# Kernel tuning notes

Hardware: AMD Instinct MI355X
Metric: run time of the kernel (lower is better)

Reference implementation:

```python
import jax, jax.numpy as jnp
import numpy as np

GROUPS = 8
EPS = 1e-5


def group_norm_dim1(x, gamma, beta):
    # Faithful to torch: GroupNorm treats dim 1 (height) as the channel axis.
    B, H, W, C = x.shape
    xg = x.reshape(B, GROUPS, H // GROUPS, W, C)
    mean = xg.mean(axis=(2, 3, 4), keepdims=True)
    var = xg.var(axis=(2, 3, 4), keepdims=True)
    xn = ((xg - mean) * jax.lax.rsqrt(var + EPS)).reshape(B, H, W, C)
    return xn * gamma[None, :, None, None] + beta[None, :, None, None]


def setup_inputs() -> dict:
    key = jax.random.key(0)
    ks = jax.random.split(key, 8)
    B, H, W, C = 4, 64, 64, 64  # height must equal units for GroupNorm to apply
    s = 1.0 / np.sqrt(C)
    return {
        "x": jax.random.normal(ks[0], (B, H, W, C), dtype=jnp.float32),
        "gamma": jnp.ones((C,), jnp.float32),
        "beta": jnp.zeros((C,), jnp.float32),
        "Wq": jax.random.normal(ks[1], (C, C), jnp.float32) * s,
        "bq": jnp.zeros((C,), jnp.float32),
        "Wk": jax.random.normal(ks[2], (C, C), jnp.float32) * s,
        "bk": jnp.zeros((C,), jnp.float32),
        "Wv": jax.random.normal(ks[3], (C, C), jnp.float32) * s,
        "bv": jnp.zeros((C,), jnp.float32),
        "Wo": jax.random.normal(ks[4], (C, C), jnp.float32) * s,
        "bo": jnp.zeros((C,), jnp.float32),
    }


def reference(x, gamma, beta, Wq, bq, Wk, bk, Wv, bv, Wo, bo):
    B, H, W, C = x.shape
    scale = C ** (-0.5)
    xn = group_norm_dim1(x, gamma, beta)
    q = xn @ Wq + bq
    k = xn @ Wk + bk
    v = xn @ Wv + bv
    # full spatial self-attention: scores [B, H, W, H*W]
    scores = jnp.einsum('bhwc,bijc->bhwij', q, k) * scale
    attn = jax.nn.softmax(scores.reshape(B, H, W, H * W), axis=-1)
    attn = attn.reshape(B, H, W, H, W)
    proj = jnp.einsum('bhwij,bijc->bhwc', attn, v)
    proj = proj @ Wo + bo
    return xn + proj
```

## Files before the change

### kernel.cpp

```cpp
#include <hip/hip_runtime.h>

typedef __bf16 bf16_t;
typedef bf16_t bf16x8 __attribute__((ext_vector_type(8)));
typedef bf16_t bf16x4 __attribute__((ext_vector_type(4)));
typedef short  short4v __attribute__((ext_vector_type(4)));
typedef float  f32x4  __attribute__((ext_vector_type(4)));

#define MFMA32(a, b, c) __builtin_amdgcn_mfma_f32_16x16x32_bf16(a, b, c, 0, 0, 0)
#define MFMA16(a, b, c) __builtin_amdgcn_mfma_f32_16x16x16bf16_1k(a, b, c, 0, 0, 0)

__global__ __launch_bounds__(256) void gn1w_kernel(const float* __restrict__ x,
    float2* __restrict__ partials,
    const float* __restrict__ Wq, const float* __restrict__ Wk,
    const float* __restrict__ Wv, const float* __restrict__ Wo,
    bf16_t* __restrict__ Wt) {
  int blk = blockIdx.x, t = threadIdx.x;
  if (blk >= 256) {
    int idx = (blk - 256) * 256 + t;
    int wsel = idx >> 12, rem = idx & 4095;
    int c = rem >> 6, kk = rem & 63;
    const float* src = (wsel == 0) ? Wq : ((wsel == 1) ? Wk : ((wsel == 2) ? Wv : Wo));
    Wt[idx] = (bf16_t)src[kk * 64 + c];
    return;
  }
  const float4* x4 = (const float4*)x + (size_t)blk * 1024;
  float s = 0.f, sq = 0.f;
  #pragma unroll
  for (int u = 0; u < 4; ++u) {
    float4 v = x4[u * 256 + t];
    s  += v.x + v.y + v.z + v.w;
    sq += v.x * v.x + v.y * v.y + v.z * v.z + v.w * v.w;
  }
  for (int off = 32; off; off >>= 1) {
    s  += __shfl_down(s, off, 64);
    sq += __shfl_down(sq, off, 64);
  }
  __shared__ float2 ps[4];
  if ((t & 63) == 0) ps[t >> 6] = make_float2(s, sq);
  __syncthreads();
  if (t == 0) {
    float S = 0.f, Q = 0.f;
    #pragma unroll
    for (int i = 0; i < 4; ++i) { S += ps[i].x; Q += ps[i].y; }
    partials[blk] = make_float2(S, Q);
  }
}

__global__ __launch_bounds__(256) void gnqkv_kernel(
    const float* __restrict__ x, const float* __restrict__ gamma,
    const float* __restrict__ beta, const float2* __restrict__ parts,
    const bf16_t* __restrict__ Wt,
    const float* __restrict__ bq, const float* __restrict__ bk, const float* __restrict__ bv,
    bf16_t* __restrict__ xnb, bf16_t* __restrict__ qo, bf16_t* __restrict__ ko,
    bf16_t* __restrict__ vo) {
  __shared__ __align__(16) bf16_t xl[4096];
  int blk = blockIdx.x, t = threadIdx.x;
  int grp = blk >> 3;
  float S = 0.f, Q = 0.f;
  #pragma unroll
  for (int i = 0; i < 8; ++i) { float2 p = parts[grp * 8 + i]; S += p.x; Q += p.y; }
  float mean = S * (1.f / 32768.f);
  float rstd = rsqrtf(Q * (1.f / 32768.f) - mean * mean + 1e-5f);
  int h = blk & 63;
  float ga = gamma[h] * rstd;
  float be = beta[h] - mean * ga;
  {
    int r = t >> 2, col0 = (t & 3) * 16;
    const float4* x4 = (const float4*)(x + (size_t)blk * 4096 + r * 64 + col0);
    bf16x8 pk0, pk1;
    float4 v0 = x4[0], v1 = x4[1], v2 = x4[2], v3 = x4[3];
    pk0[0] = (bf16_t)(v0.x * ga + be); pk0[1] = (bf16_t)(v0.y * ga + be);
    pk0[2] = (bf16_t)(v0.z * ga + be); pk0[3] = (bf16_t)(v0.w * ga + be);
    pk0[4] = (bf16_t)(v1.x * ga + be); pk0[5] = (bf16_t)(v1.y * ga + be);
    pk0[6] = (bf16_t)(v1.z * ga + be); pk0[7] = (bf16_t)(v1.w * ga + be);
    pk1[0] = (bf16_t)(v2.x * ga + be); pk1[1] = (bf16_t)(v2.y * ga + be);
    pk1[2] = (bf16_t)(v2.z * ga + be); pk1[3] = (bf16_t)(v2.w * ga + be);
    pk1[4] = (bf16_t)(v3.x * ga + be); pk1[5] = (bf16_t)(v3.y * ga + be);
    pk1[6] = (bf16_t)(v3.z * ga + be); pk1[7] = (bf16_t)(v3.w * ga + be);
    *(bf16x8*)&xnb[(size_t)blk * 4096 + r * 64 + col0]     = pk0;
    *(bf16x8*)&xnb[(size_t)blk * 4096 + r * 64 + col0 + 8] = pk1;
    int sw = r & 7, j0 = (t & 3) * 2;
    *(bf16x8*)&xl[r * 64 + ((j0 ^ sw) << 3)]       = pk0;
    *(bf16x8*)&xl[r * 64 + (((j0 + 1) ^ sw) << 3)] = pk1;
  }
  __syncthreads();
  int w = t >> 6, lane = t & 63, quad = lane >> 4, l16 = lane & 15;
  int rl = w * 16 + l16, sw2 = rl & 7;
  bf16x8 a0 = *(const bf16x8*)&xl[rl * 64 + ((quad ^ sw2) << 3)];
  bf16x8 a1 = *(const bf16x8*)&xl[rl * 64 + (((quad + 4) ^ sw2) << 3)];
  int m0 = blk * 64 + w * 16;
  int bi = m0 >> 12, kk0 = (m0 & 4095) + quad * 4;
  f32x4 zero = {0.f, 0.f, 0.f, 0.f};
  const float QSCALE = 0.125f * 1.44269504088896340736f;
  #pragma unroll
  for (int outk = 0; outk < 3; ++outk) {
    const bf16_t* wt = Wt + outk * 4096;
    const float* bias = (outk == 0) ? bq : ((outk == 1) ? bk : bv);
    #pragma unroll
    for (int nt = 0; nt < 4; ++nt) {
      int col = nt * 16 + l16;
      bf16x8 b0 = *(const bf16x8*)&wt[col * 64 + quad * 8];
      bf16x8 b1 = *(const bf16x8*)&wt[col * 64 + 32 + quad * 8];
      f32x4 acc = MFMA32(a0, b0, zero);
      acc = MFMA32(a1, b1, acc);
      float bb = bias[col];
      if (outk == 2) {
        bf16x4 pk;
        #pragma unroll
        for (int r = 0; r < 4; ++r) pk[r] = (bf16_t)(acc[r] + bb);
        *(bf16x4*)&vo[(size_t)bi * 262144 + (size_t)(kk0 >> 2) * 256 + col * 4] = pk;
      } else {
        #pragma unroll
        for (int r = 0; r < 4; ++r) {
          int m = m0 + quad * 4 + r;
          float v = acc[r] + bb;
          if (outk == 0) qo[(size_t)m * 64 + col] = (bf16_t)(v * QSCALE);
          else           ko[(size_t)m * 64 + col] = (bf16_t)v;
        }
      }
    }
  }
}

__global__ __launch_bounds__(256, 2) void flash_kernel(
    const bf16_t* __restrict__ q, const bf16_t* __restrict__ k,
    const bf16_t* __restrict__ vp, const bf16_t* __restrict__ Wt,
    const float* __restrict__ bo, const bf16_t* __restrict__ xnb,
    float* __restrict__ out) {
  __shared__ float redO[2][2048];
  __shared__ float redL[2][128];
  int t = threadIdx.x;
  int w = t >> 6, lane = t & 63, quad = lane >> 4, l16 = lane & 15;
  int b = blockIdx.y;
  int q0 = blockIdx.x * 32;

  bf16x8 qf[2][2];
  {
    const bf16_t* qp = q + ((size_t)b * 4096 + q0 + l16) * 64;
    #pragma unroll
    for (int qt = 0; qt < 2; ++qt)
      #pragma unroll
      for (int hh = 0; hh < 2; ++hh)
        qf[qt][hh] = *(const bf16x8*)&qp[qt * 1024 + hh * 32 + quad * 8];
  }
  f32x4 o[2][4];
  f32x4 zero = {0.f, 0.f, 0.f, 0.f};
  #pragma unroll
  for (int qt = 0; qt < 2; ++qt)
    #pragma unroll
    for (int ct = 0; ct < 4; ++ct) o[qt][ct] = zero;
  float rs[2] = {0.f, 0.f};

  const bf16_t* kbase = k  + (size_t)b * 262144;
  const bf16_t* vbase = vp + (size_t)b * 262144;
  int key00 = w * 1024;

  bf16x8 kfA[2][2], kfB[2][2];
  short4v vaA[4][2], vaB[4][2];
  #pragma unroll
  for (int kt = 0; kt < 2; ++kt) {
    #pragma unroll
    for (int hh = 0; hh < 2; ++hh)
      kfA[kt][hh] = *(const bf16x8*)&kbase[(size_t)(key00 + kt * 16 + l16) * 64 + hh * 32 + quad * 8];
    int cb = ((key00 + kt * 16) >> 2) + quad;
    #pragma unroll
    for (int ct = 0; ct < 4; ++ct)
      vaA[ct][kt] = *(const short4v*)&vbase[(size_t)cb * 256 + (ct * 16 + l16) * 4];
  }

#define FLASH_STEP(KF, VA, PRE, KFN, VAN, PKEY)                                       \
  {                                                                                   \
    if (PRE) {                                      \
      _Pragma("unroll")                                                               \
      for (int kt = 0; kt < 2; ++kt) {                                                \
        _Pragma("unroll")                                                             \
        for (int hh = 0; hh < 2; ++hh)                                                \
          KFN[kt][hh] = *(const bf16x8*)&kbase[(size_t)((PKEY) + kt * 16 + l16) * 64 + hh * 32 + quad * 8]; \
        int cb = (((PKEY) + kt * 16) >> 2) + quad;                                    \
        _Pragma("unroll")                                                             \
        for (int ct = 0; ct < 4; ++ct)                                                \
          VAN[ct][kt] = *(const short4v*)&vbase[(size_t)cb * 256 + (ct * 16 + l16) * 4]; \
      }                                                                               \
    }                                                                                 \
    _Pragma("unroll")                                                                 \
    for (int kt = 0; kt < 2; ++kt) {                                                  \
      _Pragma("unroll")                                                               \
      for (int qt = 0; qt < 2; ++qt) {                                                \
        f32x4 st = MFMA32(KF[kt][0], qf[qt][0], zero);                                \
        st = MFMA32(KF[kt][1], qf[qt][1], st);                       \
        bf16x4 pb;                                                                    \
        float psum = 0.f;                                                             \
        _Pragma("unroll")                                                             \
        for (int r = 0; r < 4; ++r) {                                                 \
          float p = __builtin_amdgcn_exp2f(st[r]);                                    \
          psum += p;                                                                  \
          pb[r] = (bf16_t)p;                                                          \
        }                                                                             \
        rs[qt] += psum;                                                               \
        short4v pshort = __builtin_bit_cast(short4v, pb);                             \
        _Pragma("unroll")                                                             \
        for (int ct = 0; ct < 4; ++ct)                                                \
          o[qt][ct] = MFMA16(VA[ct][kt], pshort, o[qt][ct]);                          \
      }                                                                               \
    }                                                                                 \
  }

  #pragma unroll 1
  for (int pair = 0; pair < 16; ++pair) {
    int key0 = key00 + pair * 64;
    FLASH_STEP(kfA, vaA, 1,           kfB, vaB, key0 + 32);
    FLASH_STEP(kfB, vaB, (pair < 15), kfA, vaA, key0 + 64);
  }
#undef FLASH_STEP

  #pragma unroll
  for (int qt = 0; qt < 2; ++qt) {
    rs[qt] += __shfl_xor(rs[qt], 16, 64);
    rs[qt] += __shfl_xor(rs[qt], 32, 64);
  }
  if (w >= 2) {
    int buf = w - 2;
    #pragma unroll
    for (int qt = 0; qt < 2; ++qt) {
      #pragma unroll
      for (int ct = 0; ct < 4; ++ct)
        #pragma unroll
        for (int r = 0; r < 4; ++r)
          redO[buf][((qt * 4 + ct) * 4 + r) * 64 + lane] = o[qt][ct][r];
      redL[buf][qt * 64 + lane] = rs[qt];
    }
  }
  __syncthreads();
  if (w < 2) {
    #pragma unroll
    for (int qt = 0; qt < 2; ++qt) {
      #pragma unroll
      for (int ct = 0; ct < 4; ++ct)
        #pragma unroll
        for (int r = 0; r < 4; ++r)
          o[qt][ct][r] += redO[w][((qt * 4 + ct) * 4 + r) * 64 + lane];
      rs[qt] += redL[w][qt * 64 + lane];
    }
  }
  __syncthreads();
  if (w == 0) {
    #pragma unroll
    for (int ct = 0; ct < 4; ++ct)
      #pragma unroll
      for (int r = 0; r < 4; ++r)
        redO[0][(ct * 4 + r) * 64 + lane] = o[1][ct][r];
    redL[0][lane] = rs[1];
  } else if (w == 1) {
    #pragma unroll
    for (int ct = 0; ct < 4; ++ct)
      #pragma unroll
      for (int r = 0; r < 4; ++r)
        redO[1][(ct * 4 + r) * 64 + lane] = o[0][ct][r];
    redL[1][lane] = rs[0];
  }
  __syncthreads();
  if (w < 2) {
    int myqt = w, ob = w ^ 1;
    float lt = rs[myqt] + redL[ob][lane];
    float linv = 1.f / lt;
    short4v obf[4];
    #pragma unroll
    for (int ct = 0; ct < 4; ++ct) {
      bf16x4 tb;
      #pragma unroll
      for (int r = 0; r < 4; ++r)
        tb[r] = (bf16_t)((o[myqt][ct][r] + redO[ob][(ct * 4 + r) * 64 + lane]) * linv);
      obf[ct] = __builtin_bit_cast(short4v, tb);
    }
    const bf16_t* wt3 = Wt + 3 * 4096;
    int qg = b * 4096 + q0 + myqt * 16 + l16;
    #pragma unroll
    for (int cpt = 0; cpt < 4; ++cpt) {
      f32x4 acc = zero;
      #pragma unroll
      for (int ct = 0; ct < 4; ++ct) {
        short4v wa = *(const short4v*)&wt3[(cpt * 16 + l16) * 64 + ct * 16 + quad * 4];
        acc = MFMA16(wa, obf[ct], acc);
      }
      int c0 = cpt * 16 + quad * 4;
      #pragma unroll
      for (int r = 0; r < 4; ++r) {
        int cc = c0 + r;
        size_t off = (size_t)qg * 64 + cc;
        out[off] = acc[r] + bo[cc] + (float)xnb[off];
      }
    }
  }
}

extern "C" void kernel_launch(void* const* d_in, const int* in_sizes, int n_in,
                              void* d_out, int out_size, void* d_ws, size_t ws_size,
                              hipStream_t stream) {
  const float* x     = (const float*)d_in[0];
  const float* gamma = (const float*)d_in[1];
  const float* beta  = (const float*)d_in[2];
  const float* Wq    = (const float*)d_in[3];
  const float* bq    = (const float*)d_in[4];
  const float* Wk    = (const float*)d_in[5];
  const float* bk    = (const float*)d_in[6];
  const float* Wv    = (const float*)d_in[7];
  const float* bv    = (const float*)d_in[8];
  const float* Wo    = (const float*)d_in[9];
  const float* bo    = (const float*)d_in[10];
  float* out = (float*)d_out;

  char* ws = (char*)d_ws;
  bf16_t* xnb   = (bf16_t*)(ws + 0);
  bf16_t* qb    = (bf16_t*)(ws + (2u  << 20));
  bf16_t* kb    = (bf16_t*)(ws + (4u  << 20));
  bf16_t* vb    = (bf16_t*)(ws + (6u  << 20));
  float2* parts = (float2*)(ws + (8u  << 20));
  bf16_t* Wt    = (bf16_t*)(ws + (8u  << 20) + 4096);

  hipLaunchKernelGGL(gn1w_kernel,  dim3(320),    dim3(256), 0, stream, x, parts, Wq, Wk, Wv, Wo, Wt);
  hipLaunchKernelGGL(gnqkv_kernel, dim3(256),    dim3(256), 0, stream, x, gamma, beta, parts, Wt, bq, bk, bv, xnb, qb, kb, vb);
  hipLaunchKernelGGL(flash_kernel, dim3(128, 4), dim3(256), 0, stream, qb, kb, vb, Wt, bo, xnb, out);
}
```

Baseline: 141.2 us.

## Relayout V into 64-key blocks and load 64-key tiles per flash step

Changes the V workspace layout so each 64-key block stores, per channel, contiguous keys. This lets the flash kernel fetch V with 16-byte loads instead of 8-byte ones. Each flash step now processes 64 keys instead of 32, with K and V prefetch double-buffered at that granularity. The grid is also transposed so adjacent blocks belong to different batches, which changes L2 locality. The wider register buffers raise VGPR pressure under launch_bounds(256,2).

```diff
diff --git a/kernel.cpp b/kernel.cpp
--- a/kernel.cpp
+++ b/kernel.cpp
@@ -4,6 +4,7 @@
 typedef bf16_t bf16x8 __attribute__((ext_vector_type(8)));
 typedef bf16_t bf16x4 __attribute__((ext_vector_type(4)));
 typedef short  short4v __attribute__((ext_vector_type(4)));
+typedef short  short8v __attribute__((ext_vector_type(8)));
 typedef float  f32x4  __attribute__((ext_vector_type(4)));
 
 #define MFMA32(a, b, c) __builtin_amdgcn_mfma_f32_16x16x32_bf16(a, b, c, 0, 0, 0)
@@ -89,7 +90,7 @@
   bf16x8 a0 = *(const bf16x8*)&xl[rl * 64 + ((quad ^ sw2) << 3)];
   bf16x8 a1 = *(const bf16x8*)&xl[rl * 64 + (((quad + 4) ^ sw2) << 3)];
   int m0 = blk * 64 + w * 16;
-  int bi = m0 >> 12, kk0 = (m0 & 4095) + quad * 4;
+  int bi = m0 >> 12;
   f32x4 zero = {0.f, 0.f, 0.f, 0.f};
   const float QSCALE = 0.125f * 1.44269504088896340736f;
   #pragma unroll
@@ -108,7 +109,8 @@
         bf16x4 pk;
         #pragma unroll
         for (int r = 0; r < 4; ++r) pk[r] = (bf16_t)(acc[r] + bb);
-        *(bf16x4*)&vo[(size_t)bi * 262144 + (size_t)(kk0 >> 2) * 256 + col * 4] = pk;
+        *(bf16x4*)&vo[(size_t)bi * 262144 + (size_t)(blk & 63) * 4096
+                      + (size_t)col * 64 + quad * 16 + w * 4] = pk;
       } else {
         #pragma unroll
         for (int r = 0; r < 4; ++r) {
@@ -131,8 +133,8 @@
   __shared__ float redL[2][128];
   int t = threadIdx.x;
   int w = t >> 6, lane = t & 63, quad = lane >> 4, l16 = lane & 15;
-  int b = blockIdx.y;
-  int q0 = blockIdx.x * 32;
+  int b = blockIdx.x;
+  int q0 = blockIdx.y * 32;
 
   bf16x8 qf[2][2];
   {
@@ -155,35 +157,39 @@
   const bf16_t* vbase = vp + (size_t)b * 262144;
   int key00 = w * 1024;
 
-  bf16x8 kfA[2][2], kfB[2][2];
-  short4v vaA[4][2], vaB[4][2];
-  #pragma unroll
-  for (int kt = 0; kt < 2; ++kt) {
+  bf16x8 kfA[4][2], kfB[4][2];
+  bf16x8 vaA[4][2], vaB[4][2];
+  #pragma unroll
+  for (int kt = 0; kt < 4; ++kt)
     #pragma unroll
     for (int hh = 0; hh < 2; ++hh)
       kfA[kt][hh] = *(const bf16x8*)&kbase[(size_t)(key00 + kt * 16 + l16) * 64 + hh * 32 + quad * 8];
-    int cb = ((key00 + kt * 16) >> 2) + quad;
+  {
+    const bf16_t* vg = vbase + (size_t)(key00 >> 6) * 4096 + quad * 16;
     #pragma unroll
     for (int ct = 0; ct < 4; ++ct)
-      vaA[ct][kt] = *(const short4v*)&vbase[(size_t)cb * 256 + (ct * 16 + l16) * 4];
+      #pragma unroll
+      for (int hh = 0; hh < 2; ++hh)
+        vaA[ct][hh] = *(const bf16x8*)&vg[(ct * 16 + l16) * 64 + hh * 8];
   }
 
 #define FLASH_STEP(KF, VA, PRE, KFN, VAN, PKEY)                                       \
   {                                                                                   \
-    if (PRE) {                                      \
+    if (PRE) {                               \
       _Pragma("unroll")                                                               \
-      for (int kt = 0; kt < 2; ++kt) {                                                \
+      for (int kt = 0; kt < 4; ++kt)                                                  \
         _Pragma("unroll")                                                             \
         for (int hh = 0; hh < 2; ++hh)                                                \
           KFN[kt][hh] = *(const bf16x8*)&kbase[(size_t)((PKEY) + kt * 16 + l16) * 64 + hh * 32 + quad * 8]; \
-        int cb = (((PKEY) + kt * 16) >> 2) + quad;                                    \
+      const bf16_t* vg = vbase + (size_t)((PKEY) >> 6) * 4096 + quad * 16;            \
+      _Pragma("unroll")                                                               \
+      for (int ct = 0; ct < 4; ++ct)                                                  \
         _Pragma("unroll")                                                             \
-        for (int ct = 0; ct < 4; ++ct)                                                \
-          VAN[ct][kt] = *(const short4v*)&vbase[(size_t)cb * 256 + (ct * 16 + l16) * 4]; \
-      }                                                                               \
+        for (int hh = 0; hh < 2; ++hh)                                                \
+          VAN[ct][hh] = *(const bf16x8*)&vg[(ct * 16 + l16) * 64 + hh * 8];           \
     }                                                                                 \
     _Pragma("unroll")                                                                 \
-    for (int kt = 0; kt < 2; ++kt) {                                                  \
+    for (int kt = 0; kt < 4; ++kt) {                                                  \
       _Pragma("unroll")                                                               \
       for (int qt = 0; qt < 2; ++qt) {                                                \
         f32x4 st = MFMA32(KF[kt][0], qf[qt][0], zero);                                \
@@ -199,17 +205,21 @@
         rs[qt] += psum;                                                               \
         short4v pshort = __builtin_bit_cast(short4v, pb);                             \
         _Pragma("unroll")                                                             \
-        for (int ct = 0; ct < 4; ++ct)                                                \
-          o[qt][ct] = MFMA16(VA[ct][kt], pshort, o[qt][ct]);                          \
+        for (int ct = 0; ct < 4; ++ct) {                                              \
+          short8v vv = __builtin_bit_cast(short8v, VA[ct][kt >> 1]);                  \
+          short4v vh = (kt & 1) ? __builtin_shufflevector(vv, vv, 4, 5, 6, 7)         \
+                                : __builtin_shufflevector(vv, vv, 0, 1, 2, 3);        \
+          o[qt][ct] = MFMA16(vh, pshort, o[qt][ct]);                                  \
+        }                                                                             \
       }                                                                               \
     }                                                                                 \
   }
 
   #pragma unroll 1
-  for (int pair = 0; pair < 16; ++pair) {
-    int key0 = key00 + pair * 64;
-    FLASH_STEP(kfA, vaA, 1,           kfB, vaB, key0 + 32);
-    FLASH_STEP(kfB, vaB, (pair < 15), kfA, vaA, key0 + 64);
+  for (int pair = 0; pair < 8; ++pair) {
+    int key0 = key00 + pair * 128;
+    FLASH_STEP(kfA, vaA, 1,          kfB, vaB, key0 + 64);
+    FLASH_STEP(kfB, vaB, (pair < 7), kfA, vaA, key0 + 128);
   }
 #undef FLASH_STEP
 
@@ -319,5 +329,5 @@
 
   hipLaunchKernelGGL(gn1w_kernel,  dim3(320),    dim3(256), 0, stream, x, parts, Wq, Wk, Wv, Wo, Wt);
   hipLaunchKernelGGL(gnqkv_kernel, dim3(256),    dim3(256), 0, stream, x, gamma, beta, parts, Wt, bq, bk, bv, xnb, qb, kb, vb);
-  hipLaunchKernelGGL(flash_kernel, dim3(128, 4), dim3(256), 0, stream, qb, kb, vb, Wt, bo, xnb, out);
+  hipLaunchKernelGGL(flash_kernel, dim3(4, 128), dim3(256), 0, stream, qb, kb, vb, Wt, bo, xnb, out);
 }
```

Result: slower. 154.4 us (+9.4%).
